# Performance work log

Hardware: AMD Instinct MI355X
Metric: run time of the kernel (lower is better)

Reference implementation:

```python
import jax, jax.numpy as jnp
import numpy as np

B, L1, L2, H = 16, 2048, 2048, 768


def setup_inputs() -> dict:
    key = jax.random.key(0)
    k1, k2, k3 = jax.random.split(key, 3)
    hi1 = jax.random.normal(k1, (B, L1, H), dtype=jnp.float32)
    hi2 = jax.random.normal(k2, (B, L2, H), dtype=jnp.float32)
    # xavier_uniform: bound = sqrt(6/(H+H))
    bound = float(np.sqrt(6.0 / (H + H)))
    wg = jax.random.uniform(k3, (H, H), dtype=jnp.float32, minval=-bound, maxval=bound)
    return {"hi1": hi1, "hi2": hi2, "wg": wg}


def reference(hi1, hi2, wg):
    # G = (hi1 @ wg) @ hi2^T  -> [B, L1, L2]
    g = jnp.einsum('bik,kl->bil', hi1, wg)
    scores = jnp.einsum('bil,bjl->bij', g, hi2)
    attn = jax.nn.softmax(scores, axis=2)
    # weighted sum over hi2 -> [B, L1, H]
    return jnp.einsum('bij,bjh->bih', attn, hi2)
```

## Files before the change

kernel.cpp:

```cpp
#include <hip/hip_runtime.h>
#include <hip/hip_bf16.h>

#define BB  16
#define LL1 2048
#define LL2 2048
#define HH  768

typedef __attribute__((ext_vector_type(4))) float f32x4;
typedef __attribute__((ext_vector_type(8))) _Float16 f16x8;
typedef __attribute__((ext_vector_type(4))) _Float16 f16x4;

typedef __attribute__((address_space(3))) unsigned int lds_uint;
typedef __attribute__((address_space(1))) const unsigned int glob_uint;
__device__ __forceinline__ void gl_lds16(const void* g, void* l) {
  __builtin_amdgcn_global_load_lds((glob_uint*)g, (lds_uint*)l, 16, 0, 0);
}

__global__ __launch_bounds__(256) void k_split16(
    const float* __restrict__ in, _Float16* __restrict__ p, int n4)
{
  int i = blockIdx.x * 256 + threadIdx.x;
  int stride = gridDim.x * 256;
  for (; i < n4; i += stride) {
    f32x4 v = ((const f32x4*)in)[i];
    f16x4 o;
#pragma unroll
    for (int q = 0; q < 4; ++q) o[q] = (_Float16)v[q];
    ((f16x4*)p)[i] = o;
  }
}

__global__ __launch_bounds__(256) void k_split_wt16(
    const float* __restrict__ wg, _Float16* __restrict__ wt)
{
  __shared__ float t[32][33];
  const int k0 = blockIdx.y * 32, n0 = blockIdx.x * 32;
  const int tx = threadIdx.x & 31, ty = threadIdx.x >> 5;
#pragma unroll
  for (int r = ty; r < 32; r += 8) t[r][tx] = wg[(size_t)(k0 + r) * HH + n0 + tx];
  __syncthreads();
#pragma unroll
  for (int r = ty; r < 32; r += 8)
    wt[(size_t)(n0 + r) * HH + k0 + tx] = (_Float16)t[tx][r];
}


#define STAGE_PAIR(buf, koff)                                              \
  do {                                                                     \
    gl_lds16(pA + goA[0] + (koff), (char*)&sA[buf][0] + lo0);              \
    gl_lds16(pA + goA[1] + (koff), (char*)&sA[buf][0] + lo1);              \
    gl_lds16(pB + goB[0] + (koff), (char*)&sB[buf][0] + lo0);              \
    gl_lds16(pB + goB[1] + (koff), (char*)&sB[buf][0] + lo1);              \
  } while (0)

#define KLOOP_2PHASE(NT)                                                   \
  STAGE_PAIR(0, 0);                                                        \
  asm volatile("s_waitcnt vmcnt(0)" ::: "memory");                         \
  __builtin_amdgcn_s_barrier();                                            \
  __builtin_amdgcn_sched_barrier(0);                                       \
  for (int t = 0; t < (NT); ++t) {                                         \
    const int cur = t & 1;                                                 \
    if (t < (NT) - 1) STAGE_PAIR(cur ^ 1, (t + 1) * 32);                   \
    f16x8 fa[4], fb[4];                                                    \
    _Pragma("unroll")                                                      \
    for (int mi = 0; mi < 4; ++mi) {                                       \
      int r = wm + mi * 16 + fr;                                           \
      int kb = (kg * 2) ^ ((r & 3) << 4);                                  \
      fa[mi] = *(const f16x8*)((const char*)&sA[cur][0] + r * 64 + kb);    \
    }                                                                      \
    _Pragma("unroll")                                                      \
    for (int ni = 0; ni < 4; ++ni) {                                       \
      int r = wn + ni * 16 + fr;                                           \
      int kb = (kg * 2) ^ ((r & 3) << 4);                                  \
      fb[ni] = *(const f16x8*)((const char*)&sB[cur][0] + r * 64 + kb);    \
    }                                                                      \
    _Pragma("unroll")                                                      \
    for (int mi = 0; mi < 4; ++mi)                                         \
      _Pragma("unroll")                                                    \
      for (int ni = 0; ni < 4; ++ni)                                       \
        acc[mi][ni] = __builtin_amdgcn_mfma_f32_16x16x32_f16(              \
            fa[mi], fb[ni], acc[mi][ni], 0, 0, 0);                         \
    asm volatile("s_waitcnt vmcnt(0)" ::: "memory");                       \
    __builtin_amdgcn_s_barrier();                                          \
    __builtin_amdgcn_sched_barrier(0);                                     \
  }

#define STAGE_ADDR_SETUP()                                                 \
  size_t goA[2], goB[2];                                                   \
  int lo0, lo1;                                                            \
  {                                                                        \
    int f0 = threadIdx.x, f1 = 256 + threadIdx.x;                          \
    int r0s = f0 >> 2, r1s = f1 >> 2;                                      \
    int c0 = ((f0 & 3) * 8) ^ ((r0s & 3) << 3);                            \
    int c1 = ((f1 & 3) * 8) ^ ((r1s & 3) << 3);                            \
    goA[0] = (size_t)r0s * HH + c0; goA[1] = (size_t)r1s * HH + c1;        \
    goB[0] = goA[0]; goB[1] = goA[1];                                      \
    lo0 = f0 * 16; lo1 = f1 * 16;                                          \
  }

__global__ __launch_bounds__(256) void k_gemm_f16(
    const _Float16* __restrict__ A, const _Float16* __restrict__ Bt,
    _Float16* __restrict__ C)
{
  __shared__ _Float16 sA[2][4096], sB[2][4096];
  const int tid = threadIdx.x, lane = tid & 63, wave = tid >> 6;
  const int wm = (wave >> 1) * 64, wn = (wave & 1) * 64;
  const int m0 = blockIdx.y * 128, n0 = blockIdx.x * 128;
  const int fr = lane & 15, kg = (lane >> 4) * 8;
  const _Float16* pA = A  + (size_t)m0 * HH;
  const _Float16* pB = Bt + (size_t)n0 * HH;
  f32x4 acc[4][4] = {};
  STAGE_ADDR_SETUP();

  KLOOP_2PHASE(24);

#pragma unroll
  for (int mi = 0; mi < 4; ++mi)
#pragma unroll
    for (int ni = 0; ni < 4; ++ni)
#pragma unroll
      for (int j = 0; j < 4; ++j) {
        int row = m0 + wm + mi * 16 + (lane >> 4) * 4 + j;
        int col = n0 + wn + ni * 16 + fr;
        C[(size_t)row * HH + col] = (_Float16)acc[mi][ni][j];
      }
}

__global__ __launch_bounds__(256) void k_scores_f16(
    const _Float16* __restrict__ G, const _Float16* __restrict__ H2,
    _Float16* __restrict__ S16, float* __restrict__ Mx, int b_base)
{
  __shared__ _Float16 sA[2][4096], sB[2][4096];
  const int tid = threadIdx.x, lane = tid & 63, wave = tid >> 6;
  const int wm = (wave >> 1) * 64, wn = (wave & 1) * 64;
  const int z = blockIdx.z, b = b_base + z;
  const int i0 = blockIdx.y * 128, j0 = blockIdx.x * 128;
  const int fr = lane & 15, kg = (lane >> 4) * 8;
  const _Float16* pA = G  + (size_t)b * LL1 * HH + (size_t)i0 * HH;
  const _Float16* pB = H2 + (size_t)b * LL2 * HH + (size_t)j0 * HH;
  _Float16* Sp = S16 + (size_t)z * LL1 * LL2;
  float* Mp = Mx + (size_t)z * LL1 * 16;
  f32x4 acc[4][4] = {};
  STAGE_ADDR_SETUP();

  KLOOP_2PHASE(24);

  __syncthreads();
  float* smax = (float*)&sA[0][0];
#pragma unroll
  for (int mi = 0; mi < 4; ++mi)
#pragma unroll
    for (int j = 0; j < 4; ++j) {
      float rm = fmaxf(fmaxf(acc[mi][0][j], acc[mi][1][j]),
                       fmaxf(acc[mi][2][j], acc[mi][3][j]));
#pragma unroll
      for (int off = 8; off >= 1; off >>= 1) rm = fmaxf(rm, __shfl_xor(rm, off));
      if ((lane & 15) == 0)
        smax[(wm + mi * 16 + (lane >> 4) * 4 + j) * 2 + (wave & 1)] = rm;
    }
  __syncthreads();

#pragma unroll
  for (int mi = 0; mi < 4; ++mi)
#pragma unroll
    for (int j = 0; j < 4; ++j) {
      int rloc = wm + mi * 16 + (lane >> 4) * 4 + j;
      float tmax = fmaxf(smax[rloc * 2], smax[rloc * 2 + 1]);
      int row = i0 + rloc;
#pragma unroll
      for (int ni = 0; ni < 4; ++ni) {
        int col = j0 + wn + ni * 16 + fr;
        float d = fmaxf(acc[mi][ni][j] - tmax, -28.0f);
        Sp[(size_t)row * LL2 + col] = (_Float16)d;
      }
    }
  if (tid < 128)
    Mp[(size_t)(i0 + tid) * 16 + (j0 >> 7)] = fmaxf(smax[tid * 2], smax[tid * 2 + 1]);
}

__global__ __launch_bounds__(512) void k_select(
    const _Float16* __restrict__ S16, const float* __restrict__ Mx,
    const _Float16* __restrict__ H2f, float* __restrict__ Out, int b_base)
{
  const int tid = threadIdx.x, lane = tid & 63, wv = tid >> 6;
  const int z = blockIdx.y, b = b_base + z;
  const int row = blockIdx.x * 4 + (wv >> 1);
  const int half = wv & 1;
  const _Float16* srow = S16 + ((size_t)z * LL1 + row) * LL2;
  const _Float16* V = H2f + (size_t)b * LL2 * HH;

  float bmax = Mx[((size_t)z * LL1 + row) * 16 + (lane & 15)];
  float m = bmax;
#pragma unroll
  for (int off = 8; off >= 1; off >>= 1) m = fmaxf(m, __shfl_xor(m, off));

  const float thr = m - 20.0f;
  float acc[6] = {};
  float lsum = 0.f;

  for (int jb = 0; jb < 16; ++jb) {
    float bj = __shfl(bmax, jb);
    if (bj <= thr) continue;
#pragma unroll
    for (int h = 0; h < 2; ++h) {
      float sval = bj + (float)srow[jb * 128 + h * 64 + lane];
      bool hit = sval > thr;
      unsigned long long mask = __ballot(hit);
      float p = hit ? __expf(sval - m) : 0.f;
      lsum += p;
      while (mask) {
        int src = __ffsll((long long)mask) - 1;
        mask &= mask - 1;
        float w = __shfl(p, src);
        int j = jb * 128 + h * 64 + src;
        const _Float16* vr = V + (size_t)j * HH + half * 384;
#pragma unroll
        for (int c = 0; c < 6; ++c) acc[c] = fmaf(w, (float)vr[lane + 64 * c], acc[c]);
      }
    }
  }
#pragma unroll
  for (int off = 32; off >= 1; off >>= 1) lsum += __shfl_xor(lsum, off);
  const float inv = 1.0f / lsum;
  float* orow = Out + ((size_t)b * LL1 + row) * HH + half * 384;
#pragma unroll
  for (int c = 0; c < 6; ++c) orow[lane + 64 * c] = acc[c] * inv;
}

extern "C" void kernel_launch(void* const* d_in, const int* in_sizes, int n_in,
                              void* d_out, int out_size, void* d_ws, size_t ws_size,
                              hipStream_t stream) {
  const float* hi1 = (const float*)d_in[0];
  const float* hi2 = (const float*)d_in[1];
  const float* wg  = (const float*)d_in[2];
  float* out = (float*)d_out;

  char* ws = (char*)d_ws;
  const size_t plane_elems = (size_t)BB * LL1 * HH;
  const size_t plane_b = plane_elems * 2;
  const size_t wt_b = (size_t)HH * HH * 2;
  const size_t s16_per_b = (size_t)LL1 * LL2 * 2;
  const size_t m_per_b = (size_t)LL1 * 16 * 4;

  _Float16* H2f = (_Float16*)ws;
  _Float16* Gf  = (_Float16*)(ws + plane_b);
  _Float16* Wtf = (_Float16*)(ws + 2 * plane_b);
  char* X = ws + 2 * plane_b + wt_b;
  _Float16* H1f = (_Float16*)X;

  const size_t fixed = 2 * plane_b + wt_b;
  int CB = 1;
  const int cand[5] = {16, 8, 4, 2, 1};
  for (int i = 0; i < 5; ++i) {
    size_t xneed = (size_t)cand[i] * (s16_per_b + m_per_b);
    if (xneed < plane_b) xneed = plane_b;
    if (fixed + xneed + 1024 <= ws_size) { CB = cand[i]; break; }
  }
  _Float16* S16 = (_Float16*)X;
  float* Mbuf = (float*)(X + (size_t)CB * s16_per_b);

  k_split16<<<4096, 256, 0, stream>>>(hi1, H1f, (int)(plane_elems / 4));
  k_split16<<<4096, 256, 0, stream>>>(hi2, H2f, (int)(plane_elems / 4));
  k_split_wt16<<<dim3(HH / 32, HH / 32), 256, 0, stream>>>(wg, Wtf);

  k_gemm_f16<<<dim3(HH / 128, (BB * LL1) / 128), 256, 0, stream>>>(H1f, Wtf, Gf);

  for (int b0 = 0; b0 < BB; b0 += CB) {
    k_scores_f16<<<dim3(LL2 / 128, LL1 / 128, CB), 256, 0, stream>>>(Gf, H2f, S16, Mbuf, b0);
    k_select<<<dim3(LL1 / 4, CB), 512, 0, stream>>>(S16, Mbuf, H2f, out, b0);
  }
}
```

Baseline: 429.4 us.

## Enlarge GEMM tiles to 256x128 with 8 waves and fully unrolled K loop

The fp16 GEMM and scores kernels move from 256-thread 128x128 tiles to 512-thread 256x128 tiles. Each of the eight waves still computes 64x64, and the B tile is now shared by twice as many rows, which cuts global and LDS traffic per output. LDS fragment offsets are precomputed outside the loop, and the 24-step K loop is fully unrolled. The trade-offs are more LDS per block, larger code and lower occupancy limits, and the scores epilogue has to handle 256 rows per block.

New measurement: 400.4 us. 6.7% less time.

```diff
diff --git a/kernel.cpp b/kernel.cpp
--- a/kernel.cpp
+++ b/kernel.cpp
@@ -5,6 +5,7 @@
 #define LL1 2048
 #define LL2 2048
 #define HH  768
+#define NT  24
 
 typedef __attribute__((ext_vector_type(4))) float f32x4;
 typedef __attribute__((ext_vector_type(8))) _Float16 f16x8;
@@ -45,74 +46,76 @@
 }
 
 
-#define STAGE_PAIR(buf, koff)                                              \
-  do {                                                                     \
-    gl_lds16(pA + goA[0] + (koff), (char*)&sA[buf][0] + lo0);              \
-    gl_lds16(pA + goA[1] + (koff), (char*)&sA[buf][0] + lo1);              \
-    gl_lds16(pB + goB[0] + (koff), (char*)&sB[buf][0] + lo0);              \
-    gl_lds16(pB + goB[1] + (koff), (char*)&sB[buf][0] + lo1);              \
-  } while (0)
-
-#define KLOOP_2PHASE(NT)                                                   \
-  STAGE_PAIR(0, 0);                                                        \
+#define STAGE_SETUP()                                                      \
+  size_t goA0, goA1, goB0; int loA0, loA1, loB0;                           \
+  {                                                                        \
+    int f0 = tid, f1 = 512 + tid;                                          \
+    int r0 = f0 >> 2, s0 = f0 & 3, r1 = f1 >> 2, s1 = f1 & 3;              \
+    goA0 = (size_t)r0 * HH + (size_t)((s0 ^ (r0 & 3)) * 8);                \
+    goA1 = (size_t)r1 * HH + (size_t)((s1 ^ (r1 & 3)) * 8);                \
+    loA0 = f0 * 16; loA1 = f1 * 16;                                        \
+    int rb = tid >> 2, sb = tid & 3;                                       \
+    goB0 = (size_t)rb * HH + (size_t)((sb ^ (rb & 3)) * 8);                \
+    loB0 = tid * 16;                                                       \
+  }                                                                        \
+  int offA[4], offB[4];                                                    \
+  _Pragma("unroll")                                                        \
+  for (int mi = 0; mi < 4; ++mi) {                                         \
+    int r = wm + mi * 16 + fr;                                             \
+    offA[mi] = r * 64 + ((l4 * 16) ^ ((r & 3) << 4));                      \
+  }                                                                        \
+  _Pragma("unroll")                                                        \
+  for (int ni = 0; ni < 4; ++ni) {                                         \
+    int r = wn + ni * 16 + fr;                                             \
+    offB[ni] = r * 64 + ((l4 * 16) ^ ((r & 3) << 4));                      \
+  }
+
+#define STG(buf, k0)                                                       \
+  gl_lds16(pA + goA0 + (k0), (char*)&sA[buf][0] + loA0);                   \
+  gl_lds16(pA + goA1 + (k0), (char*)&sA[buf][0] + loA1);                   \
+  gl_lds16(pB + goB0 + (k0), (char*)&sB[buf][0] + loB0);
+
+#define CMP(buf)                                                           \
+  {                                                                        \
+    f16x8 fa[4], fb[4];                                                    \
+    _Pragma("unroll") for (int mi = 0; mi < 4; ++mi)                       \
+      fa[mi] = *(const f16x8*)((const char*)&sA[buf][0] + offA[mi]);       \
+    _Pragma("unroll") for (int ni = 0; ni < 4; ++ni)                       \
+      fb[ni] = *(const f16x8*)((const char*)&sB[buf][0] + offB[ni]);       \
+    _Pragma("unroll") for (int mi = 0; mi < 4; ++mi)                       \
+      _Pragma("unroll") for (int ni = 0; ni < 4; ++ni)                     \
+        acc[mi][ni] = __builtin_amdgcn_mfma_f32_16x16x32_f16(              \
+            fa[mi], fb[ni], acc[mi][ni], 0, 0, 0);                         \
+  }
+
+#define KLOOP()                                                            \
+  STG(0, 0);                                                               \
   asm volatile("s_waitcnt vmcnt(0)" ::: "memory");                         \
   __builtin_amdgcn_s_barrier();                                            \
   __builtin_amdgcn_sched_barrier(0);                                       \
-  for (int t = 0; t < (NT); ++t) {                                         \
-    const int cur = t & 1;                                                 \
-    if (t < (NT) - 1) STAGE_PAIR(cur ^ 1, (t + 1) * 32);                   \
-    f16x8 fa[4], fb[4];                                                    \
-    _Pragma("unroll")                                                      \
-    for (int mi = 0; mi < 4; ++mi) {                                       \
-      int r = wm + mi * 16 + fr;                                           \
-      int kb = (kg * 2) ^ ((r & 3) << 4);                                  \
-      fa[mi] = *(const f16x8*)((const char*)&sA[cur][0] + r * 64 + kb);    \
-    }                                                                      \
-    _Pragma("unroll")                                                      \
-    for (int ni = 0; ni < 4; ++ni) {                                       \
-      int r = wn + ni * 16 + fr;                                           \
-      int kb = (kg * 2) ^ ((r & 3) << 4);                                  \
-      fb[ni] = *(const f16x8*)((const char*)&sB[cur][0] + r * 64 + kb);    \
-    }                                                                      \
-    _Pragma("unroll")                                                      \
-    for (int mi = 0; mi < 4; ++mi)                                         \
-      _Pragma("unroll")                                                    \
-      for (int ni = 0; ni < 4; ++ni)                                       \
-        acc[mi][ni] = __builtin_amdgcn_mfma_f32_16x16x32_f16(              \
-            fa[mi], fb[ni], acc[mi][ni], 0, 0, 0);                         \
+  _Pragma("unroll")                                                        \
+  for (int t = 0; t < NT; ++t) {                                           \
+    if (t < NT - 1) { STG((t + 1) & 1, (t + 1) * 32); }                    \
+    CMP(t & 1);                                                            \
     asm volatile("s_waitcnt vmcnt(0)" ::: "memory");                       \
     __builtin_amdgcn_s_barrier();                                          \
     __builtin_amdgcn_sched_barrier(0);                                     \
   }
 
-#define STAGE_ADDR_SETUP()                                                 \
-  size_t goA[2], goB[2];                                                   \
-  int lo0, lo1;                                                            \
-  {                                                                        \
-    int f0 = threadIdx.x, f1 = 256 + threadIdx.x;                          \
-    int r0s = f0 >> 2, r1s = f1 >> 2;                                      \
-    int c0 = ((f0 & 3) * 8) ^ ((r0s & 3) << 3);                            \
-    int c1 = ((f1 & 3) * 8) ^ ((r1s & 3) << 3);                            \
-    goA[0] = (size_t)r0s * HH + c0; goA[1] = (size_t)r1s * HH + c1;        \
-    goB[0] = goA[0]; goB[1] = goA[1];                                      \
-    lo0 = f0 * 16; lo1 = f1 * 16;                                          \
-  }
-
-__global__ __launch_bounds__(256) void k_gemm_f16(
+__global__ __launch_bounds__(512, 4) void k_gemm_f16(
     const _Float16* __restrict__ A, const _Float16* __restrict__ Bt,
     _Float16* __restrict__ C)
 {
-  __shared__ _Float16 sA[2][4096], sB[2][4096];
+  __shared__ _Float16 sA[2][256 * 32], sB[2][128 * 32];
   const int tid = threadIdx.x, lane = tid & 63, wave = tid >> 6;
   const int wm = (wave >> 1) * 64, wn = (wave & 1) * 64;
-  const int m0 = blockIdx.y * 128, n0 = blockIdx.x * 128;
-  const int fr = lane & 15, kg = (lane >> 4) * 8;
+  const int m0 = blockIdx.y * 256, n0 = blockIdx.x * 128;
+  const int fr = lane & 15, l4 = lane >> 4;
   const _Float16* pA = A  + (size_t)m0 * HH;
   const _Float16* pB = Bt + (size_t)n0 * HH;
   f32x4 acc[4][4] = {};
-  STAGE_ADDR_SETUP();
-
-  KLOOP_2PHASE(24);
+  STAGE_SETUP();
+  KLOOP();
 
 #pragma unroll
   for (int mi = 0; mi < 4; ++mi)
@@ -126,24 +129,23 @@
       }
 }
 
-__global__ __launch_bounds__(256) void k_scores_f16(
+__global__ __launch_bounds__(512, 4) void k_scores_f16(
     const _Float16* __restrict__ G, const _Float16* __restrict__ H2,
     _Float16* __restrict__ S16, float* __restrict__ Mx, int b_base)
 {
-  __shared__ _Float16 sA[2][4096], sB[2][4096];
+  __shared__ _Float16 sA[2][256 * 32], sB[2][128 * 32];
   const int tid = threadIdx.x, lane = tid & 63, wave = tid >> 6;
   const int wm = (wave >> 1) * 64, wn = (wave & 1) * 64;
   const int z = blockIdx.z, b = b_base + z;
-  const int i0 = blockIdx.y * 128, j0 = blockIdx.x * 128;
-  const int fr = lane & 15, kg = (lane >> 4) * 8;
+  const int i0 = blockIdx.y * 256, j0 = blockIdx.x * 128;
+  const int fr = lane & 15, l4 = lane >> 4;
   const _Float16* pA = G  + (size_t)b * LL1 * HH + (size_t)i0 * HH;
   const _Float16* pB = H2 + (size_t)b * LL2 * HH + (size_t)j0 * HH;
   _Float16* Sp = S16 + (size_t)z * LL1 * LL2;
   float* Mp = Mx + (size_t)z * LL1 * 16;
   f32x4 acc[4][4] = {};
-  STAGE_ADDR_SETUP();
-
-  KLOOP_2PHASE(24);
+  STAGE_SETUP();
+  KLOOP();
 
   __syncthreads();
   float* smax = (float*)&sA[0][0];
@@ -174,7 +176,7 @@
         Sp[(size_t)row * LL2 + col] = (_Float16)d;
       }
     }
-  if (tid < 128)
+  if (tid < 256)
     Mp[(size_t)(i0 + tid) * 16 + (j0 >> 7)] = fmaxf(smax[tid * 2], smax[tid * 2 + 1]);
 }
 
@@ -263,10 +265,10 @@
   k_split16<<<4096, 256, 0, stream>>>(hi2, H2f, (int)(plane_elems / 4));
   k_split_wt16<<<dim3(HH / 32, HH / 32), 256, 0, stream>>>(wg, Wtf);
 
-  k_gemm_f16<<<dim3(HH / 128, (BB * LL1) / 128), 256, 0, stream>>>(H1f, Wtf, Gf);
+  k_gemm_f16<<<dim3(HH / 128, (BB * LL1) / 256), 512, 0, stream>>>(H1f, Wtf, Gf);
 
   for (int b0 = 0; b0 < BB; b0 += CB) {
-    k_scores_f16<<<dim3(LL2 / 128, LL1 / 128, CB), 256, 0, stream>>>(Gf, H2f, S16, Mbuf, b0);
+    k_scores_f16<<<dim3(LL2 / 128, LL1 / 256, CB), 512, 0, stream>>>(Gf, H2f, S16, Mbuf, b0);
     k_select<<<dim3(LL1 / 4, CB), 512, 0, stream>>>(S16, Mbuf, H2f, out, b0);
   }
 }
```
